# Optimization experiments

Hardware: AMD Instinct MI355X
Metric: run time of the kernel (lower is better)

The kernel has to match this reference:

```python
import jax, jax.numpy as jnp
import numpy as np

E, H, L, HALF = 100, 256, 4, 128  # embed_dim, hidden_dim, num res blocks, hidden//2
B, A = 1024, 256                   # batch, n_actions
EPS = 1e-5                         # torch LayerNorm default eps


def _ln(x, g, b):
    m = jnp.mean(x, axis=-1, keepdims=True)
    v = jnp.var(x, axis=-1, keepdims=True)
    return (x - m) * jax.lax.rsqrt(v + EPS) * g + b


def _block(x, w, bb, g, be):
    # Linear -> ReLU -> LayerNorm (Dropout prob 0.0 == identity)
    return _ln(jax.nn.relu(x @ w + bb), g, be)


def _encode(x, w_in, b_in, g_in, be_in, Wr, Br, Gr, Ber):
    h = _block(x, w_in, b_in, g_in, be_in)
    def step(h, p):
        w, bb, g, be = p
        return h + _block(h, w, bb, g, be), None
    h, _ = jax.lax.scan(step, h, (Wr, Br, Gr, Ber))
    return h


def setup_inputs() -> dict:
    key = jax.random.key(0)
    k = jax.random.split(key, 16)
    s = 0.05
    d = {}
    d['obs_embeddings'] = jax.random.normal(k[0], (B, 1, E), jnp.float32)
    d['action_embeddings'] = jax.random.normal(k[1], (B, A, E), jnp.float32)
    mask = jax.random.randint(k[2], (B, A), 0, 2).astype(jnp.int32)
    d['action_mask'] = mask.at[:, 0].set(1)  # ensure >=1 valid action per row
    # PolicyNetwork params (weights stored [in, out])
    d['pw_in'] = jax.random.normal(k[3], (E, H), jnp.float32) * s
    d['pb_in'] = jnp.zeros((H,), jnp.float32)
    d['pg_in'] = jnp.ones((H,), jnp.float32)
    d['pbe_in'] = jnp.zeros((H,), jnp.float32)
    d['pW'] = jax.random.normal(k[4], (L, H, H), jnp.float32) * s
    d['pB'] = jnp.zeros((L, H), jnp.float32)
    d['pG'] = jnp.ones((L, H), jnp.float32)
    d['pBe'] = jnp.zeros((L, H), jnp.float32)
    d['po_w1'] = jax.random.normal(k[5], (H, H), jnp.float32) * s
    d['po_b1'] = jnp.zeros((H,), jnp.float32)
    d['po_w2'] = jax.random.normal(k[6], (H, E), jnp.float32) * s
    d['po_b2'] = jnp.zeros((E,), jnp.float32)
    # ValueNetwork params
    d['vw_in'] = jax.random.normal(k[7], (E, H), jnp.float32) * s
    d['vb_in'] = jnp.zeros((H,), jnp.float32)
    d['vg_in'] = jnp.ones((H,), jnp.float32)
    d['vbe_in'] = jnp.zeros((H,), jnp.float32)
    d['vW'] = jax.random.normal(k[8], (L, H, H), jnp.float32) * s
    d['vB'] = jnp.zeros((L, H), jnp.float32)
    d['vG'] = jnp.ones((L, H), jnp.float32)
    d['vBe'] = jnp.zeros((L, H), jnp.float32)
    d['vo_w1'] = jax.random.normal(k[9], (H, HALF), jnp.float32) * s
    d['vo_b1'] = jnp.zeros((HALF,), jnp.float32)
    d['vo_w2'] = jax.random.normal(k[10], (HALF, 1), jnp.float32) * s
    d['vo_b2'] = jnp.zeros((1,), jnp.float32)
    return d


def reference(obs_embeddings, action_embeddings, action_mask,
              pw_in, pb_in, pg_in, pbe_in, pW, pB, pG, pBe,
              po_w1, po_b1, po_w2, po_b2,
              vw_in, vb_in, vg_in, vbe_in, vW, vB, vG, vBe,
              vo_w1, vo_b1, vo_w2, vo_b2):
    mask = action_mask.astype(bool)

    def pol_encode(x2d):
        h = _encode(x2d, pw_in, pb_in, pg_in, pbe_in, pW, pB, pG, pBe)
        return jax.nn.relu(h @ po_w1 + po_b1) @ po_w2 + po_b2

    # obs: (B,1,E) -> (B,E); all items valid
    enc_obs = pol_encode(obs_embeddings.reshape(-1, E))
    # actions: mask-gather -> MLP -> scatter-back == compute-all then zero masked
    # (valid because the MLP/LayerNorm acts per-row independently)
    enc_act = pol_encode(action_embeddings.reshape(-1, E)).reshape(B, A, E)
    enc_act = enc_act * mask[..., None]
    logits = jnp.einsum('be,bae->ba', enc_obs, enc_act) / jnp.sqrt(jnp.float32(E))
    logits = jnp.where(mask, logits, -jnp.inf)

    # value net runs on raw obs embeddings
    hv = _encode(obs_embeddings.reshape(-1, E), vw_in, vb_in, vg_in, vbe_in, vW, vB, vG, vBe)
    value = (jax.nn.relu(hv @ vo_w1 + vo_b1) @ vo_w2 + vo_b2)[:, 0]
    return logits, value
```

## Files before the change

kernel.cpp:

```cpp
#include <hip/hip_runtime.h>
#include <math.h>


typedef unsigned short u16;
typedef _Float16 f16;
typedef _Float16 half8 __attribute__((ext_vector_type(8)));
typedef float floatx4 __attribute__((ext_vector_type(4)));

#define E_DIM  100
#define H_DIM  256
#define NLAYER 4
#define BATCH  1024
#define NACT   256
#define NROWS_ACT (BATCH * NACT)
#define LN_EPS 1e-5f

#define NET_WIN  0
#define NET_WL(l) (32768 + (l) * 65536)
#define NET_W1   294912
#define NET_W2P  360448
#define POL_SZ   389120
#define VAL_BASE POL_SZ
#define PACK_TOTAL (POL_SZ + 327680)

#define TROWS 32
#define ACT_BLOCKS (NROWS_ACT / TROWS)
#define OBS_BLOCKS (BATCH / TROWS)

#define WS_VROWS   16
#define WS_ENCOBS  (16 + NROWS_ACT * 4)
#define WS_PACK    (WS_ENCOBS + BATCH * E_DIM * 4)
#define WS_ENCACT  (WS_PACK + PACK_TOTAL * 2)

__device__ __forceinline__ u16 f2h_u16(float f) {
  union { u16 u; f16 h; } c; c.h = (f16)f; return c.u;
}

__device__ __forceinline__ float wsum(float v) {
#pragma unroll
  for (int off = 1; off < 64; off <<= 1) v += __shfl_xor(v, off, 64);
  return v;
}

template <int CTRL>
__device__ __forceinline__ float dpp_add(float v) {
  const int t = __builtin_amdgcn_update_dpp(0, __float_as_int(v), CTRL, 0xF, 0xF, true);
  return v + __int_as_float(t);
}
__device__ __forceinline__ float dpp_red16(float v) {
  v = dpp_add<0xB1>(v);
  v = dpp_add<0x4E>(v);
  v = dpp_add<0x141>(v);
  v = dpp_add<0x140>(v);
  return v;
}

__global__ void zero_counter_kernel(int* counter) { *counter = 0; }

__global__ void compact_kernel(const int* __restrict__ mask, int n,
                               int* __restrict__ counter,
                               int* __restrict__ rows,
                               u16* __restrict__ logits)
{
  const int i = blockIdx.x * blockDim.x + threadIdx.x;
  const int lane = threadIdx.x & 63;
  bool valid = false;
  if (i < n) {
    valid = (mask[i] != 0);
    if (!valid) logits[i] = (u16)0xFBFF;
  }
  const unsigned long long bal = __ballot(valid);
  const int cnt = __popcll(bal);
  int base = 0;
  if (lane == 0 && cnt) base = atomicAdd(counter, cnt);
  base = __shfl(base, 0, 64);
  if (valid) {
    const int off = __popcll(bal & ((1ull << lane) - 1ull));
    rows[base + off] = i;
  }
}

__device__ __forceinline__ f16 pack_elem(const f16* __restrict__ W, int li,
                                         int K, int N, int Np)
{
  const int j = li & 7, lane = (li >> 3) & 63, tile = li >> 9;
  const int ntiles = Np >> 4;
  const int k0 = (tile / ntiles) * 32, n0 = (tile % ntiles) * 16;
  const int k = k0 + ((lane >> 4) << 3) + j, n = n0 + (lane & 15);
  return (k < K && n < N) ? W[k * N + n] : (f16)0.f;
}

__global__ void pack_all_kernel(
    const f16* __restrict__ pw_in, const f16* __restrict__ pW,
    const f16* __restrict__ po_w1, const f16* __restrict__ po_w2,
    const f16* __restrict__ vw_in, const f16* __restrict__ vW,
    const f16* __restrict__ vo_w1, f16* __restrict__ dst)
{
  const int i = blockIdx.x * blockDim.x + threadIdx.x;
  if (i >= PACK_TOTAL) return;
  f16 v;
  if (i < 32768)        v = pack_elem(pw_in, i, E_DIM, H_DIM, 256);
  else if (i < 294912) { const int r = i - 32768, l = r >> 16;
                         v = pack_elem(pW + (size_t)l * 65536, r & 65535, 256, 256, 256); }
  else if (i < 360448)  v = pack_elem(po_w1, i - 294912, 256, 256, 256);
  else if (i < 389120)  v = pack_elem(po_w2, i - 360448, 256, E_DIM, 112);
  else if (i < 421888)  v = pack_elem(vw_in, i - 389120, E_DIM, H_DIM, 256);
  else if (i < 684032) { const int r = i - 421888, l = r >> 16;
                         v = pack_elem(vW + (size_t)l * 65536, r & 65535, 256, 256, 256); }
  else                  v = pack_elem(vo_w1, i - 684032, 256, 128, 128);
  dst[i] = v;
}

template <int KT, int NTC>
__device__ __forceinline__ void wave_gemm_t(
    const f16* __restrict__ pw, int ntiles_all,
    const f16* __restrict__ h16, int q, int l15, int lane,
    int nt_base, floatx4 acc0[], floatx4 acc1[])
{
  const f16* pl = pw + (size_t)nt_base * 512 + lane * 8;
  const size_t kstride = (size_t)ntiles_all * 512;
  half8 bc[NTC];
#pragma unroll
  for (int t = 0; t < NTC; ++t) bc[t] = *(const half8*)(pl + t * 512);
#pragma unroll
  for (int k = 0; k < KT; ++k) {
    half8 bn[NTC];
#pragma unroll
    for (int t = 0; t < NTC; ++t)
      if (k + 1 < KT) bn[t] = *(const half8*)(pl + (size_t)(k + 1) * kstride + t * 512);
    const half8 a0 = *(const half8*)(h16 + l15 * 264 + k * 32 + q * 8);
    const half8 a1 = *(const half8*)(h16 + (16 + l15) * 264 + k * 32 + q * 8);
#pragma unroll
    for (int t = 0; t < NTC; ++t) {
      acc0[t] = __builtin_amdgcn_mfma_f32_16x16x32_f16(a0, bc[t], acc0[t], 0, 0, 0);
      acc1[t] = __builtin_amdgcn_mfma_f32_16x16x32_f16(a1, bc[t], acc1[t], 0, 0, 0);
    }
#pragma unroll
    for (int t = 0; t < NTC; ++t)
      if (k + 1 < KT) bc[t] = bn[t];
  }
}

template <bool R16>
__device__ __forceinline__ void run_trunk(
    const f16* __restrict__ packN,
    const f16* __restrict__ b_in, const f16* __restrict__ g_in, const f16* __restrict__ be_in,
    const f16* __restrict__ Br, const f16* __restrict__ Gr, const f16* __restrict__ Ber,
    f16* __restrict__ h16, float (*red)[4][2],
    floatx4 acc[2][4], float* __restrict__ resf, f16* __restrict__ res16,
    int q, int l15, int lane, int cw, int n0)
{
#pragma unroll 1
  for (int l = 0; l <= NLAYER; ++l) {
    const f16* pw; const f16* bias; const f16* g; const f16* be;
    if (l == 0) { pw = packN + NET_WIN; bias = b_in; g = g_in; be = be_in; }
    else {
      pw = packN + NET_WL(l - 1); bias = Br + (l - 1) * H_DIM;
      g = Gr + (l - 1) * H_DIM;   be = Ber + (l - 1) * H_DIM;
    }
#pragma unroll
    for (int t = 0; t < 4; ++t) {
      const float bv = (float)bias[n0 + t * 16 + l15];
      acc[0][t] = (floatx4){bv, bv, bv, bv};
      acc[1][t] = acc[0][t];
    }
    if (l == 0) wave_gemm_t<4, 4>(pw, 16, h16, q, l15, lane, cw * 4, acc[0], acc[1]);
    else        wave_gemm_t<8, 4>(pw, 16, h16, q, l15, lane, cw * 4, acc[0], acc[1]);

#pragma unroll
    for (int mt = 0; mt < 2; ++mt)
#pragma unroll
      for (int reg = 0; reg < 4; ++reg) {
        float s = 0.f, s2 = 0.f;
#pragma unroll
        for (int t = 0; t < 4; ++t) {
          const float v = fmaxf(acc[mt][t][reg], 0.f);
          acc[mt][t][reg] = v;
          s += v; s2 += v * v;
        }
        s  = dpp_red16(s);
        s2 = dpp_red16(s2);
        if (l15 == 0) {
          const int R = mt * 16 + q * 4 + reg;
          red[R][cw][0] = s; red[R][cw][1] = s2;
        }
      }
    __syncthreads();

#pragma unroll
    for (int mt = 0; mt < 2; ++mt)
#pragma unroll
      for (int reg = 0; reg < 4; ++reg) {
        const int R = mt * 16 + q * 4 + reg;
        const float s  = red[R][0][0] + red[R][1][0] + red[R][2][0] + red[R][3][0];
        const float s2 = red[R][0][1] + red[R][1][1] + red[R][2][1] + red[R][3][1];
        const float mean = s * (1.f / 256.f);
        const float var  = s2 * (1.f / 256.f) - mean * mean;
        const float rstd = 1.f / sqrtf(var + LN_EPS);
#pragma unroll
        for (int t = 0; t < 4; ++t) {
          const int col = n0 + t * 16 + l15;
          const int ri = (mt * 4 + t) * 4 + reg;
          const float v = (acc[mt][t][reg] - mean) * rstd *
                          (float)g[col] + (float)be[col];
          float rprev;
          if (l == 0) rprev = 0.f;
          else rprev = R16 ? (float)res16[ri] : resf[ri];
          const float r = rprev + v;
          if (R16) res16[ri] = (f16)r; else resf[ri] = r;
          h16[R * 264 + col] = (f16)r;
        }
      }
    __syncthreads();
  }
}

__device__ __forceinline__ void policy_heads(
    const f16* __restrict__ packN,
    const f16* __restrict__ b1, const f16* __restrict__ b2,
    f16* __restrict__ h16, floatx4 acc[2][4],
    int q, int l15, int lane, int cw, int n0)
{
#pragma unroll
  for (int t = 0; t < 4; ++t) {
    const float bv = (float)b1[n0 + t * 16 + l15];
    acc[0][t] = (floatx4){bv, bv, bv, bv};
    acc[1][t] = acc[0][t];
  }
  wave_gemm_t<8, 4>(packN + NET_W1, 16, h16, q, l15, lane, cw * 4, acc[0], acc[1]);
  __syncthreads();
#pragma unroll
  for (int mt = 0; mt < 2; ++mt)
#pragma unroll
    for (int reg = 0; reg < 4; ++reg) {
      const int R = mt * 16 + q * 4 + reg;
#pragma unroll
      for (int t = 0; t < 4; ++t)
        h16[R * 264 + n0 + t * 16 + l15] = (f16)fmaxf(acc[mt][t][reg], 0.f);
    }
  __syncthreads();

  const int nt_base = cw * 2;
  const int ntc = (cw < 3) ? 2 : 1;
#pragma unroll
  for (int t = 0; t < 2; ++t) {
    const int col = (nt_base + t) * 16 + l15;
    const float bv = (t < ntc && col < E_DIM) ? (float)b2[col] : 0.f;
    acc[0][t] = (floatx4){bv, bv, bv, bv};
    acc[1][t] = acc[0][t];
  }
  if (cw < 3)
    wave_gemm_t<8, 2>(packN + NET_W2P, 7, h16, q, l15, lane, nt_base, acc[0], acc[1]);
  else
    wave_gemm_t<8, 1>(packN + NET_W2P, 7, h16, q, l15, lane, nt_base, acc[0], acc[1]);
  __syncthreads();

  float* encf = (float*)h16;
#pragma unroll
  for (int mt = 0; mt < 2; ++mt)
#pragma unroll
    for (int reg = 0; reg < 4; ++reg) {
      const int R = mt * 16 + q * 4 + reg;
#pragma unroll
      for (int t = 0; t < 2; ++t)
        if (t < ntc)
          encf[R * 112 + (nt_base + t) * 16 + l15] = acc[mt][t][reg];
    }
  __syncthreads();
}

__global__ __launch_bounds__(256, 4)
void trunk_kernel(
    const f16* __restrict__ obs, const f16* __restrict__ xact,
    const int* __restrict__ vrows, const int* __restrict__ counter,
    const f16* __restrict__ packP, const f16* __restrict__ packV,
    const f16* __restrict__ pb_in, const f16* __restrict__ pg_in, const f16* __restrict__ pbe_in,
    const f16* __restrict__ pB, const f16* __restrict__ pG, const f16* __restrict__ pBe,
    const f16* __restrict__ po_b1, const f16* __restrict__ po_b2,
    const f16* __restrict__ vb_in, const f16* __restrict__ vg_in, const f16* __restrict__ vbe_in,
    const f16* __restrict__ vB, const f16* __restrict__ vG, const f16* __restrict__ vBe,
    const f16* __restrict__ vo_b1, const f16* __restrict__ vo_b2, const f16* __restrict__ vo_w2,
    float* __restrict__ enc_obs_out, f16* __restrict__ enc_act_out,
    u16* __restrict__ value_out)
{
  __shared__ __align__(16) f16 h16[TROWS * 264];
  __shared__ float red[TROWS][4][2];

  const int tid  = threadIdx.x;
  const int lane = tid & 63;
  const int w    = tid >> 6;
  const int l15 = lane & 15, q = lane >> 4;
  const int cw = w, n0 = cw * 64;

  floatx4 acc[2][4];

  if (blockIdx.x >= 2 * OBS_BLOCKS) {
    const int count = *counter;
    const int base = (blockIdx.x - 2 * OBS_BLOCKS) * TROWS;
    if (base >= count) return;

    for (int idx = tid; idx < TROWS * 128; idx += 256) {
      const int r = idx >> 7, c = idx & 127;
      const int gr = base + r;
      f16 v = (f16)0.f;
      if (c < E_DIM && gr < count) v = xact[(size_t)vrows[gr] * E_DIM + c];
      h16[r * 264 + c] = v;
    }
    __syncthreads();

    f16 res16[32];
    run_trunk<true>(packP, pb_in, pg_in, pbe_in, pB, pG, pBe, h16, red,
                    acc, nullptr, res16, q, l15, lane, cw, n0);
    policy_heads(packP, po_b1, po_b2, h16, acc, q, l15, lane, cw, n0);

    const float* encf = (const float*)h16;
    for (int idx = tid; idx < TROWS * 112; idx += 256) {
      const int r = idx / 112, c = idx - r * 112;
      enc_act_out[(size_t)(base + r) * 112 + c] = (f16)encf[r * 112 + c];
    }
    return;
  }

  const bool isv = blockIdx.x >= OBS_BLOCKS;
  const int base = (isv ? (blockIdx.x - OBS_BLOCKS) : blockIdx.x) * TROWS;

  for (int idx = tid; idx < TROWS * 128; idx += 256) {
    const int r = idx >> 7, c = idx & 127;
    h16[r * 264 + c] = (c < E_DIM) ? obs[(size_t)(base + r) * E_DIM + c] : (f16)0.f;
  }
  __syncthreads();

  if (!isv) {
    f16 res16[32];
    run_trunk<true>(packP, pb_in, pg_in, pbe_in, pB, pG, pBe, h16, red,
                    acc, nullptr, res16, q, l15, lane, cw, n0);
    policy_heads(packP, po_b1, po_b2, h16, acc, q, l15, lane, cw, n0);
    const float* encf = (const float*)h16;
    for (int idx = tid; idx < TROWS * E_DIM; idx += 256) {
      const int r = idx / E_DIM, c = idx - r * E_DIM;
      enc_obs_out[(size_t)(base + r) * E_DIM + c] = encf[r * 112 + c];
    }
  } else {
    float resf[32];
    run_trunk<false>(packV, vb_in, vg_in, vbe_in, vB, vG, vBe, h16, red,
                     acc, resf, nullptr, q, l15, lane, cw, n0);
#pragma unroll
    for (int t = 0; t < 2; ++t) {
      const float bv = (float)vo_b1[cw * 32 + t * 16 + l15];
      acc[0][t] = (floatx4){bv, bv, bv, bv};
      acc[1][t] = acc[0][t];
    }
    wave_gemm_t<8, 2>(packV + NET_W1, 8, h16, q, l15, lane, cw * 2, acc[0], acc[1]);
    __syncthreads();
    float* encf = (float*)h16;
#pragma unroll
    for (int mt = 0; mt < 2; ++mt)
#pragma unroll
      for (int reg = 0; reg < 4; ++reg) {
        const int R = mt * 16 + q * 4 + reg;
#pragma unroll
        for (int t = 0; t < 2; ++t)
          encf[R * 128 + cw * 32 + t * 16 + l15] = fmaxf(acc[mt][t][reg], 0.f);
      }
    __syncthreads();
    const float w2a = (float)vo_w2[lane], w2b = (float)vo_w2[lane + 64];
    const float b2v = (float)vo_b2[0];
    for (int j = 0; j < 8; ++j) {
      const int r = w * 8 + j;
      const float p = encf[r * 128 + lane] * w2a + encf[r * 128 + lane + 64] * w2b;
      const float tot = wsum(p);
      if (lane == 0) value_out[base + r] = f2h_u16(tot + b2v);
    }
  }
}

__global__ __launch_bounds__(256)
void logits_kernel(const int* __restrict__ vrows, const int* __restrict__ counter,
                   const f16* __restrict__ enc_act, const float* __restrict__ enc_obs,
                   u16* __restrict__ logits)
{
  const int count = *counter;
  const int lane = threadIdx.x & 63;
  const int nw = (gridDim.x * blockDim.x) >> 6;
  for (int gr = (blockIdx.x * blockDim.x + threadIdx.x) >> 6; gr < count; gr += nw) {
    const int vrow = vrows[gr];
    const int bb = vrow >> 8;
    const float* ob = enc_obs + (size_t)bb * E_DIM;
    const f16*   ar = enc_act + (size_t)gr * 112;
    float p = (float)ar[lane] * ob[lane];
    if (lane + 64 < E_DIM) p += (float)ar[lane + 64] * ob[lane + 64];
    const float tot = wsum(p);
    if (lane == 0) logits[vrow] = f2h_u16(tot * 0.1f);
  }
}

extern "C" void kernel_launch(void* const* d_in, const int* in_sizes, int n_in,
                              void* d_out, int out_size, void* d_ws, size_t ws_size,
                              hipStream_t stream)
{
  const f16* obs   = (const f16*)d_in[0];
  const f16* actE  = (const f16*)d_in[1];
  const int* mask  = (const int*)d_in[2];
  const f16* pw_in = (const f16*)d_in[3];
  const f16* pb_in = (const f16*)d_in[4];
  const f16* pg_in = (const f16*)d_in[5];
  const f16* pbe_in= (const f16*)d_in[6];
  const f16* pW    = (const f16*)d_in[7];
  const f16* pB    = (const f16*)d_in[8];
  const f16* pG    = (const f16*)d_in[9];
  const f16* pBe   = (const f16*)d_in[10];
  const f16* po_w1 = (const f16*)d_in[11];
  const f16* po_b1 = (const f16*)d_in[12];
  const f16* po_w2 = (const f16*)d_in[13];
  const f16* po_b2 = (const f16*)d_in[14];
  const f16* vw_in = (const f16*)d_in[15];
  const f16* vb_in = (const f16*)d_in[16];
  const f16* vg_in = (const f16*)d_in[17];
  const f16* vbe_in= (const f16*)d_in[18];
  const f16* vW    = (const f16*)d_in[19];
  const f16* vB    = (const f16*)d_in[20];
  const f16* vG    = (const f16*)d_in[21];
  const f16* vBe   = (const f16*)d_in[22];
  const f16* vo_w1 = (const f16*)d_in[23];
  const f16* vo_b1 = (const f16*)d_in[24];
  const f16* vo_w2 = (const f16*)d_in[25];
  const f16* vo_b2 = (const f16*)d_in[26];

  u16* logits = (u16*)d_out;
  u16* value  = (u16*)d_out + NROWS_ACT;

  int*   counter = (int*)d_ws;
  int*   vrows   = (int*)((char*)d_ws + WS_VROWS);
  float* enc_obs = (float*)((char*)d_ws + WS_ENCOBS);
  f16*   packW   = (f16*)((char*)d_ws + WS_PACK);
  f16*   enc_act = (f16*)((char*)d_ws + WS_ENCACT);

  zero_counter_kernel<<<1, 1, 0, stream>>>(counter);
  compact_kernel<<<NROWS_ACT / 256, 256, 0, stream>>>(mask, NROWS_ACT, counter,
                                                      vrows, logits);
  pack_all_kernel<<<(PACK_TOTAL + 255) / 256, 256, 0, stream>>>(
      pw_in, pW, po_w1, po_w2, vw_in, vW, vo_w1, packW);

  trunk_kernel<<<ACT_BLOCKS + 2 * OBS_BLOCKS, 256, 0, stream>>>(
      obs, actE, vrows, counter, packW, packW + VAL_BASE,
      pb_in, pg_in, pbe_in, pB, pG, pBe, po_b1, po_b2,
      vb_in, vg_in, vbe_in, vB, vG, vBe, vo_b1, vo_b2, vo_w2,
      enc_obs, enc_act, value);

  logits_kernel<<<2048, 256, 0, stream>>>(vrows, counter, enc_act, enc_obs, logits);
}
```

Measured before the change: 522.5 us.

## Split trunk work across eight waves per block with centralized LayerNorm stats

The trunk kernel moves from 256 to 512 threads per block, so each wave computes 32 output columns instead of 64. This halves per-thread accumulator and residual register state and raises the number of waves available to hide latency. LayerNorm row statistics are now reduced once per row by a single thread and stored in shared memory, at the cost of an extra barrier per layer. The head GEMMs are also redistributed across 7-8 waves, which leaves one wave idle in the policy output projection.

```diff
diff --git a/kernel.cpp b/kernel.cpp
--- a/kernel.cpp
+++ b/kernel.cpp
@@ -111,14 +111,14 @@
   dst[i] = v;
 }
 
-template <int KT, int NTC>
+template <int KT, int NTC, int NTA>
 __device__ __forceinline__ void wave_gemm_t(
-    const f16* __restrict__ pw, int ntiles_all,
-    const f16* __restrict__ h16, int q, int l15, int lane,
-    int nt_base, floatx4 acc0[], floatx4 acc1[])
+    const f16* __restrict__ pw, const f16* __restrict__ h16,
+    int q, int l15, int lane, int nt_base,
+    floatx4 acc0[], floatx4 acc1[])
 {
   const f16* pl = pw + (size_t)nt_base * 512 + lane * 8;
-  const size_t kstride = (size_t)ntiles_all * 512;
+  const size_t kstride = (size_t)NTA * 512;
   half8 bc[NTC];
 #pragma unroll
   for (int t = 0; t < NTC; ++t) bc[t] = *(const half8*)(pl + t * 512);
@@ -146,9 +146,9 @@
     const f16* __restrict__ packN,
     const f16* __restrict__ b_in, const f16* __restrict__ g_in, const f16* __restrict__ be_in,
     const f16* __restrict__ Br, const f16* __restrict__ Gr, const f16* __restrict__ Ber,
-    f16* __restrict__ h16, float (*red)[4][2],
-    floatx4 acc[2][4], float* __restrict__ resf, f16* __restrict__ res16,
-    int q, int l15, int lane, int cw, int n0)
+    f16* __restrict__ h16, float2 (*red)[8], float2* __restrict__ stats,
+    floatx4 acc[2][2], float* __restrict__ resf, f16* __restrict__ res16,
+    int tid, int q, int l15, int w, int n0)
 {
 #pragma unroll 1
   for (int l = 0; l <= NLAYER; ++l) {
@@ -159,56 +159,57 @@
       g = Gr + (l - 1) * H_DIM;   be = Ber + (l - 1) * H_DIM;
     }
 #pragma unroll
-    for (int t = 0; t < 4; ++t) {
+    for (int t = 0; t < 2; ++t) {
       const float bv = (float)bias[n0 + t * 16 + l15];
       acc[0][t] = (floatx4){bv, bv, bv, bv};
       acc[1][t] = acc[0][t];
     }
-    if (l == 0) wave_gemm_t<4, 4>(pw, 16, h16, q, l15, lane, cw * 4, acc[0], acc[1]);
-    else        wave_gemm_t<8, 4>(pw, 16, h16, q, l15, lane, cw * 4, acc[0], acc[1]);
+    if (l == 0) wave_gemm_t<4, 2, 16>(pw, h16, q, l15, tid & 63, w * 2, acc[0], acc[1]);
+    else        wave_gemm_t<8, 2, 16>(pw, h16, q, l15, tid & 63, w * 2, acc[0], acc[1]);
 
 #pragma unroll
     for (int mt = 0; mt < 2; ++mt)
 #pragma unroll
       for (int reg = 0; reg < 4; ++reg) {
-        float s = 0.f, s2 = 0.f;
-#pragma unroll
-        for (int t = 0; t < 4; ++t) {
-          const float v = fmaxf(acc[mt][t][reg], 0.f);
-          acc[mt][t][reg] = v;
-          s += v; s2 += v * v;
-        }
-        s  = dpp_red16(s);
-        s2 = dpp_red16(s2);
-        if (l15 == 0) {
-          const int R = mt * 16 + q * 4 + reg;
-          red[R][cw][0] = s; red[R][cw][1] = s2;
-        }
+        const float v0 = fmaxf(acc[mt][0][reg], 0.f);
+        const float v1 = fmaxf(acc[mt][1][reg], 0.f);
+        acc[mt][0][reg] = v0; acc[mt][1][reg] = v1;
+        float s  = dpp_red16(v0 + v1);
+        float s2 = dpp_red16(v0 * v0 + v1 * v1);
+        if (l15 == 0) red[mt * 16 + q * 4 + reg][w] = (float2){s, s2};
       }
     __syncthreads();
 
+    if (tid < TROWS) {
+      const float4* rp = (const float4*)&red[tid][0];
+      const float4 r0 = rp[0], r1 = rp[1], r2 = rp[2], r3 = rp[3];
+      const float s  = r0.x + r0.z + r1.x + r1.z + r2.x + r2.z + r3.x + r3.z;
+      const float s2 = r0.y + r0.w + r1.y + r1.w + r2.y + r2.w + r3.y + r3.w;
+      const float mean = s * (1.f / 256.f);
+      const float var  = s2 * (1.f / 256.f) - mean * mean;
+      stats[tid] = (float2){mean, 1.f / sqrtf(var + LN_EPS)};
+    }
+    __syncthreads();
+
+    const float gf0 = (float)g[n0 + l15],       gf1 = (float)g[n0 + 16 + l15];
+    const float bf0 = (float)be[n0 + l15],      bf1 = (float)be[n0 + 16 + l15];
 #pragma unroll
     for (int mt = 0; mt < 2; ++mt)
 #pragma unroll
       for (int reg = 0; reg < 4; ++reg) {
         const int R = mt * 16 + q * 4 + reg;
-        const float s  = red[R][0][0] + red[R][1][0] + red[R][2][0] + red[R][3][0];
-        const float s2 = red[R][0][1] + red[R][1][1] + red[R][2][1] + red[R][3][1];
-        const float mean = s * (1.f / 256.f);
-        const float var  = s2 * (1.f / 256.f) - mean * mean;
-        const float rstd = 1.f / sqrtf(var + LN_EPS);
-#pragma unroll
-        for (int t = 0; t < 4; ++t) {
-          const int col = n0 + t * 16 + l15;
-          const int ri = (mt * 4 + t) * 4 + reg;
-          const float v = (acc[mt][t][reg] - mean) * rstd *
-                          (float)g[col] + (float)be[col];
+        const float2 st = stats[R];
+#pragma unroll
+        for (int t = 0; t < 2; ++t) {
+          const int ri = (mt * 2 + t) * 4 + reg;
+          const float vv = (acc[mt][t][reg] - st.x) * st.y *
+                           (t == 0 ? gf0 : gf1) + (t == 0 ? bf0 : bf1);
           float rprev;
           if (l == 0) rprev = 0.f;
           else rprev = R16 ? (float)res16[ri] : resf[ri];
-          const float r = rprev + v;
+          const float r = rprev + vv;
           if (R16) res16[ri] = (f16)r; else resf[ri] = r;
-          h16[R * 264 + col] = (f16)r;
+          h16[R * 264 + n0 + t * 16 + l15] = (f16)r;
         }
       }
     __syncthreads();
@@ -218,16 +219,16 @@
 __device__ __forceinline__ void policy_heads(
     const f16* __restrict__ packN,
     const f16* __restrict__ b1, const f16* __restrict__ b2,
-    f16* __restrict__ h16, floatx4 acc[2][4],
-    int q, int l15, int lane, int cw, int n0)
-{
-#pragma unroll
-  for (int t = 0; t < 4; ++t) {
+    f16* __restrict__ h16, floatx4 acc[2][2],
+    int tid, int q, int l15, int w, int n0)
+{
+#pragma unroll
+  for (int t = 0; t < 2; ++t) {
     const float bv = (float)b1[n0 + t * 16 + l15];
     acc[0][t] = (floatx4){bv, bv, bv, bv};
     acc[1][t] = acc[0][t];
   }
-  wave_gemm_t<8, 4>(packN + NET_W1, 16, h16, q, l15, lane, cw * 4, acc[0], acc[1]);
+  wave_gemm_t<8, 2, 16>(packN + NET_W1, h16, q, l15, tid & 63, w * 2, acc[0], acc[1]);
   __syncthreads();
 #pragma unroll
   for (int mt = 0; mt < 2; ++mt)
@@ -235,41 +236,34 @@
     for (int reg = 0; reg < 4; ++reg) {
       const int R = mt * 16 + q * 4 + reg;
 #pragma unroll
-      for (int t = 0; t < 4; ++t)
+      for (int t = 0; t < 2; ++t)
         h16[R * 264 + n0 + t * 16 + l15] = (f16)fmaxf(acc[mt][t][reg], 0.f);
     }
   __syncthreads();
 
-  const int nt_base = cw * 2;
-  const int ntc = (cw < 3) ? 2 : 1;
-#pragma unroll
-  for (int t = 0; t < 2; ++t) {
-    const int col = (nt_base + t) * 16 + l15;
-    const float bv = (t < ntc && col < E_DIM) ? (float)b2[col] : 0.f;
-    acc[0][t] = (floatx4){bv, bv, bv, bv};
-    acc[1][t] = acc[0][t];
-  }
-  if (cw < 3)
-    wave_gemm_t<8, 2>(packN + NET_W2P, 7, h16, q, l15, lane, nt_base, acc[0], acc[1]);
-  else
-    wave_gemm_t<8, 1>(packN + NET_W2P, 7, h16, q, l15, lane, nt_base, acc[0], acc[1]);
+  if (w < 7) {
+    const int col = w * 16 + l15;
+    const float bv = (col < E_DIM) ? (float)b2[col] : 0.f;
+    acc[0][0] = (floatx4){bv, bv, bv, bv};
+    acc[1][0] = acc[0][0];
+    wave_gemm_t<8, 1, 7>(packN + NET_W2P, h16, q, l15, tid & 63, w, acc[0], acc[1]);
+  }
   __syncthreads();
 
   float* encf = (float*)h16;
-#pragma unroll
-  for (int mt = 0; mt < 2; ++mt)
-#pragma unroll
-    for (int reg = 0; reg < 4; ++reg) {
-      const int R = mt * 16 + q * 4 + reg;
-#pragma unroll
-      for (int t = 0; t < 2; ++t)
-        if (t < ntc)
-          encf[R * 112 + (nt_base + t) * 16 + l15] = acc[mt][t][reg];
-    }
+  if (w < 7) {
+#pragma unroll
+    for (int mt = 0; mt < 2; ++mt)
+#pragma unroll
+      for (int reg = 0; reg < 4; ++reg) {
+        const int R = mt * 16 + q * 4 + reg;
+        encf[R * 112 + w * 16 + l15] = acc[mt][0][reg];
+      }
+  }
   __syncthreads();
 }
 
-__global__ __launch_bounds__(256, 4)
+__global__ __launch_bounds__(512, 8)
 void trunk_kernel(
     const f16* __restrict__ obs, const f16* __restrict__ xact,
     const int* __restrict__ vrows, const int* __restrict__ counter,
@@ -284,22 +278,23 @@
     u16* __restrict__ value_out)
 {
   __shared__ __align__(16) f16 h16[TROWS * 264];
-  __shared__ float red[TROWS][4][2];
+  __shared__ __align__(16) float2 red[TROWS][8];
+  __shared__ float2 stats[TROWS];
 
   const int tid  = threadIdx.x;
   const int lane = tid & 63;
   const int w    = tid >> 6;
   const int l15 = lane & 15, q = lane >> 4;
-  const int cw = w, n0 = cw * 64;
-
-  floatx4 acc[2][4];
+  const int n0 = w * 32;
+
+  floatx4 acc[2][2];
 
   if (blockIdx.x >= 2 * OBS_BLOCKS) {
     const int count = *counter;
     const int base = (blockIdx.x - 2 * OBS_BLOCKS) * TROWS;
     if (base >= count) return;
 
-    for (int idx = tid; idx < TROWS * 128; idx += 256) {
+    for (int idx = tid; idx < TROWS * 128; idx += 512) {
       const int r = idx >> 7, c = idx & 127;
       const int gr = base + r;
       f16 v = (f16)0.f;
@@ -308,13 +303,13 @@
     }
     __syncthreads();
 
-    f16 res16[32];
-    run_trunk<true>(packP, pb_in, pg_in, pbe_in, pB, pG, pBe, h16, red,
-                    acc, nullptr, res16, q, l15, lane, cw, n0);
-    policy_heads(packP, po_b1, po_b2, h16, acc, q, l15, lane, cw, n0);
+    f16 res16[16];
+    run_trunk<true>(packP, pb_in, pg_in, pbe_in, pB, pG, pBe, h16, red, stats,
+                    acc, nullptr, res16, tid, q, l15, w, n0);
+    policy_heads(packP, po_b1, po_b2, h16, acc, tid, q, l15, w, n0);
 
     const float* encf = (const float*)h16;
-    for (int idx = tid; idx < TROWS * 112; idx += 256) {
+    for (int idx = tid; idx < TROWS * 112; idx += 512) {
       const int r = idx / 112, c = idx - r * 112;
       enc_act_out[(size_t)(base + r) * 112 + c] = (f16)encf[r * 112 + c];
     }
@@ -324,33 +319,32 @@
   const bool isv = blockIdx.x >= OBS_BLOCKS;
   const int base = (isv ? (blockIdx.x - OBS_BLOCKS) : blockIdx.x) * TROWS;
 
-  for (int idx = tid; idx < TROWS * 128; idx += 256) {
+  for (int idx = tid; idx < TROWS * 128; idx += 512) {
     const int r = idx >> 7, c = idx & 127;
     h16[r * 264 + c] = (c < E_DIM) ? obs[(size_t)(base + r) * E_DIM + c] : (f16)0.f;
   }
   __syncthreads();
 
   if (!isv) {
-    f16 res16[32];
-    run_trunk<true>(packP, pb_in, pg_in, pbe_in, pB, pG, pBe, h16, red,
-                    acc, nullptr, res16, q, l15, lane, cw, n0);
-    policy_heads(packP, po_b1, po_b2, h16, acc, q, l15, lane, cw, n0);
+    f16 res16[16];
+    run_trunk<true>(packP, pb_in, pg_in, pbe_in, pB, pG, pBe, h16, red, stats,
+                    acc, nullptr, res16, tid, q, l15, w, n0);
+    policy_heads(packP, po_b1, po_b2, h16, acc, tid, q, l15, w, n0);
     const float* encf = (const float*)h16;
-    for (int idx = tid; idx < TROWS * E_DIM; idx += 256) {
+    for (int idx = tid; idx < TROWS * E_DIM; idx += 512) {
       const int r = idx / E_DIM, c = idx - r * E_DIM;
       enc_obs_out[(size_t)(base + r) * E_DIM + c] = encf[r * 112 + c];
     }
   } else {
-    float resf[32];
-    run_trunk<false>(packV, vb_in, vg_in, vbe_in, vB, vG, vBe, h16, red,
-                     acc, resf, nullptr, q, l15, lane, cw, n0);
-#pragma unroll
-    for (int t = 0; t < 2; ++t) {
-      const float bv = (float)vo_b1[cw * 32 + t * 16 + l15];
-      acc[0][t] = (floatx4){bv, bv, bv, bv};
-      acc[1][t] = acc[0][t];
-    }
-    wave_gemm_t<8, 2>(packV + NET_W1, 8, h16, q, l15, lane, cw * 2, acc[0], acc[1]);
+    float resf[16];
+    run_trunk<false>(packV, vb_in, vg_in, vbe_in, vB, vG, vBe, h16, red, stats,
+                     acc, resf, nullptr, tid, q, l15, w, n0);
+    {
+      const float bv = (float)vo_b1[w * 16 + l15];
+      acc[0][0] = (floatx4){bv, bv, bv, bv};
+      acc[1][0] = acc[0][0];
+    }
+    wave_gemm_t<8, 1, 8>(packV + NET_W1, h16, q, l15, lane, w, acc[0], acc[1]);
     __syncthreads();
     float* encf = (float*)h16;
 #pragma unroll
@@ -358,15 +352,13 @@
 #pragma unroll
       for (int reg = 0; reg < 4; ++reg) {
         const int R = mt * 16 + q * 4 + reg;
-#pragma unroll
-        for (int t = 0; t < 2; ++t)
-          encf[R * 128 + cw * 32 + t * 16 + l15] = fmaxf(acc[mt][t][reg], 0.f);
+        encf[R * 128 + w * 16 + l15] = fmaxf(acc[mt][0][reg], 0.f);
       }
     __syncthreads();
     const float w2a = (float)vo_w2[lane], w2b = (float)vo_w2[lane + 64];
     const float b2v = (float)vo_b2[0];
-    for (int j = 0; j < 8; ++j) {
-      const int r = w * 8 + j;
+    for (int j = 0; j < 4; ++j) {
+      const int r = w * 4 + j;
       const float p = encf[r * 128 + lane] * w2a + encf[r * 128 + lane + 64] * w2b;
       const float tot = wsum(p);
       if (lane == 0) value_out[base + r] = f2h_u16(tot + b2v);
@@ -441,7 +433,7 @@
   pack_all_kernel<<<(PACK_TOTAL + 255) / 256, 256, 0, stream>>>(
       pw_in, pW, po_w1, po_w2, vw_in, vW, vo_w1, packW);
 
-  trunk_kernel<<<ACT_BLOCKS + 2 * OBS_BLOCKS, 256, 0, stream>>>(
+  trunk_kernel<<<ACT_BLOCKS + 2 * OBS_BLOCKS, 512, 0, stream>>>(
       obs, actE, vrows, counter, packW, packW + VAL_BASE,
       pb_in, pg_in, pbe_in, pB, pG, pBe, po_b1, po_b2,
       vb_in, vg_in, vbe_in, vB, vG, vBe, vo_b1, vo_b2, vo_w2,
```

After: 548.0 us. 4.9% more time.
